# Kernel optimization log

Measured on AMD Instinct MI355X. Metric: run time of the kernel, lower is better.

Reference implementation:

```python
import jax, jax.numpy as jnp
import numpy as np
from jax import lax

B, T = 2, 2
BT = B * T
C = 256
NH, DH = 8, 32
NL, NP = 3, 4
NLAYERS = 6
DFF = 1024
SHAPES = [(16, 16), (32, 32), (64, 64)]  # coarse -> fine, last is finest
STARTS = [0, 256, 1280]
LQ = 5376
H4 = W4 = 128
EPS = 1e-5


def setup_inputs():
    key = jax.random.key(0)
    ks = iter(jax.random.split(key, 64))
    def nrm(shape, s=0.02):
        return jax.random.normal(next(ks), shape, jnp.float32) * s
    inp = {}
    for l, (H, W) in enumerate(SHAPES):
        inp[f"src{l}"] = jax.random.normal(next(ks), (BT, C, H, W), jnp.float32)
        inp[f"pos{l}"] = jax.random.normal(next(ks), (BT, C, H, W), jnp.float32)
    inp["mask_features"] = jax.random.normal(next(ks), (B, C, T, H4, W4), jnp.float32)
    inp["level_embed"] = nrm((NL, C), 1.0)
    inp["off_w"] = nrm((NLAYERS, C, NH * NL * NP * 2), 0.01)
    inp["off_b"] = nrm((NLAYERS, NH * NL * NP * 2), 0.1)
    inp["aw_w"] = nrm((NLAYERS, C, NH * NL * NP))
    inp["aw_b"] = jnp.zeros((NLAYERS, NH * NL * NP), jnp.float32)
    inp["val_w"] = nrm((NLAYERS, C, C), 0.05)
    inp["val_b"] = jnp.zeros((NLAYERS, C), jnp.float32)
    inp["out_w"] = nrm((NLAYERS, C, C), 0.05)
    inp["out_b"] = jnp.zeros((NLAYERS, C), jnp.float32)
    inp["ln1_g"] = jnp.ones((NLAYERS, C), jnp.float32)
    inp["ln1_b"] = jnp.zeros((NLAYERS, C), jnp.float32)
    inp["ff1_w"] = nrm((NLAYERS, C, DFF))
    inp["ff1_b"] = jnp.zeros((NLAYERS, DFF), jnp.float32)
    inp["ff2_w"] = nrm((NLAYERS, DFF, C))
    inp["ff2_b"] = jnp.zeros((NLAYERS, C), jnp.float32)
    inp["ln2_g"] = jnp.ones((NLAYERS, C), jnp.float32)
    inp["ln2_b"] = jnp.zeros((NLAYERS, C), jnp.float32)
    inp["lat_w"] = nrm((NLAYERS, C, C, 1, 1), 0.05)
    inp["lat_b"] = jnp.zeros((NLAYERS, C), jnp.float32)
    inp["outc_w"] = nrm((NLAYERS, C, C, 3, 3), 0.02)
    inp["outc_b"] = jnp.zeros((NLAYERS, C), jnp.float32)
    return inp


def _ln(x, g, b):
    m = x.mean(-1, keepdims=True)
    v = ((x - m) ** 2).mean(-1, keepdims=True)
    return (x - m) * lax.rsqrt(v + EPS) * g + b


def _conv(x, w, b, pad):
    y = lax.conv_general_dilated(x, w, (1, 1), [(pad, pad), (pad, pad)],
                                 dimension_numbers=("NCHW", "OIHW", "NCHW"))
    return y + b[None, :, None, None]


def _sample_level(v_l, loc, H, W):
    # v_l: (BT, NH, H*W, DH); loc: (BT, LQ, NH, NP, 2) normalized [0,1]
    # grid_sample bilinear, align_corners=False, zero padding:
    # pixel coord = loc * size - 0.5
    bt, nh, _, dh = v_l.shape
    x = loc[..., 0] * W - 0.5
    y = loc[..., 1] * H - 0.5
    x0 = jnp.floor(x)
    y0 = jnp.floor(y)
    x0i = x0.astype(jnp.int32)
    y0i = y0.astype(jnp.int32)
    fx = (x - x0).transpose(0, 2, 1, 3)[..., None]  # (BT,NH,LQ,NP,1)
    fy = (y - y0).transpose(0, 2, 1, 3)[..., None]
    def gather(ix, iy):
        valid = (ix >= 0) & (ix < W) & (iy >= 0) & (iy < H)
        idx = jnp.clip(iy, 0, H - 1) * W + jnp.clip(ix, 0, W - 1)
        idx = idx.transpose(0, 2, 1, 3)  # (BT,NH,LQ,NP)
        Lq, P = idx.shape[2], idx.shape[3]
        g = jnp.take_along_axis(v_l, idx.reshape(bt, nh, Lq * P)[..., None], axis=2)
        g = g.reshape(bt, nh, Lq, P, dh)
        return g * valid.transpose(0, 2, 1, 3)[..., None]
    v00 = gather(x0i, y0i)
    v01 = gather(x0i + 1, y0i)
    v10 = gather(x0i, y0i + 1)
    v11 = gather(x0i + 1, y0i + 1)
    return (v00 * (1 - fx) * (1 - fy) + v01 * fx * (1 - fy)
            + v10 * (1 - fx) * fy + v11 * fx * fy)


def _ref_points():
    pts = []
    for (H, W) in SHAPES:
        ys = (jnp.arange(H, dtype=jnp.float32) + 0.5) / H
        xs = (jnp.arange(W, dtype=jnp.float32) + 0.5) / W
        gy, gx = jnp.meshgrid(ys, xs, indexing="ij")
        pts.append(jnp.stack([gx.reshape(-1), gy.reshape(-1)], -1))
    return jnp.concatenate(pts, 0)  # (LQ, 2); valid_ratios are all ones


def reference(src0, src1, src2, pos0, pos1, pos2, mask_features, level_embed,
              off_w, off_b, aw_w, aw_b, val_w, val_b, out_w, out_b,
              ln1_g, ln1_b, ff1_w, ff1_b, ff2_w, ff2_b, ln2_g, ln2_b,
              lat_w, lat_b, outc_w, outc_b):
    srcs = [src0, src1, src2]
    poss = [pos0, pos1, pos2]
    output = jnp.concatenate([s.reshape(BT, C, -1).transpose(0, 2, 1) for s in srcs], 1)
    posf = jnp.concatenate(
        [p.reshape(BT, C, -1).transpose(0, 2, 1) + level_embed[l][None, None]
         for l, p in enumerate(poss)], 1)
    refp = _ref_points()
    norm = jnp.array([[W, H] for (H, W) in SHAPES], jnp.float32)  # (NL,2) as (W,H)
    lh, lw = SHAPES[-1]
    for i in range(NLAYERS):
        q = output + posf
        v = (output @ val_w[i] + val_b[i]).reshape(BT, LQ, NH, DH)
        off = (q @ off_w[i] + off_b[i]).reshape(BT, LQ, NH, NL, NP, 2)
        aw = jax.nn.softmax((q @ aw_w[i] + aw_b[i]).reshape(BT, LQ, NH, NL * NP), -1)
        aw = aw.reshape(BT, LQ, NH, NL, NP)
        loc = refp[None, :, None, None, None, :] + off / norm[None, None, None, :, None, :]
        acc = jnp.zeros((BT, NH, LQ, DH), output.dtype)
        for l, (H, W) in enumerate(SHAPES):
            v_l = v[:, STARTS[l]:STARTS[l] + H * W].transpose(0, 2, 1, 3)
            s = _sample_level(v_l, loc[:, :, :, l], H, W)
            acc = acc + (s * aw[:, :, :, l].transpose(0, 2, 1, 3)[..., None]).sum(3)
        attn = acc.transpose(0, 2, 1, 3).reshape(BT, LQ, C) @ out_w[i] + out_b[i]
        output = _ln(output + attn, ln1_g[i], ln1_b[i])
        ff = jax.nn.relu(output @ ff1_w[i] + ff1_b[i]) @ ff2_w[i] + ff2_b[i]
        output = _ln(output + ff, ln2_g[i], ln2_b[i])
        # FPN fusion with the finest transformer level
        lm = output[:, STARTS[-1]:].reshape(BT, lh, lw, C).transpose(0, 3, 1, 2)
        x = mask_features.transpose(0, 2, 1, 3, 4).reshape(B * T, C, H4, W4)
        x = _conv(x, lat_w[i], lat_b[i], 0)
        x = x + jax.image.resize(lm, (BT, C, H4, W4), method="bilinear")
        x = jax.nn.relu(_conv(x, outc_w[i], outc_b[i], 1))
        mask_features = mask_features + x.reshape(B, T, C, H4, W4).transpose(0, 2, 1, 3, 4)
    return output, mask_features
```

## Files before the change

kernel.cpp:

```cpp
#include <hip/hip_runtime.h>

#define DEV __device__ __forceinline__

using f32x4  = __attribute__((ext_vector_type(4))) float;
using bf16x8 = __attribute__((ext_vector_type(8))) short;

static constexpr int kLQ = 5376;

DEV unsigned short f2b(float f) {
  unsigned u = __builtin_bit_cast(unsigned, f);
  u = u + 0x7fffu + ((u >> 16) & 1u);
  return (unsigned short)(u >> 16);
}
DEV float b2f(unsigned short s) {
  unsigned u = ((unsigned)s) << 16;
  return __builtin_bit_cast(float, u);
}

DEV void glds16(const void* g, void* l) {
  __builtin_amdgcn_global_load_lds(
      (const __attribute__((address_space(1))) void*)g,
      (__attribute__((address_space(3))) void*)l, 16, 0, 0);
}

template<int EPI>
__global__ __launch_bounds__(256) void gemm128(
    const unsigned short* __restrict__ A, const unsigned short* __restrict__ Bt,
    const float* __restrict__ bias, void* __restrict__ Cp,
    int M, int N, int K, const float* __restrict__ rsrc)
{
  __shared__ unsigned short As[128 * 32];
  __shared__ unsigned short Bs[128 * 32];
  const int tid = threadIdx.x, lane = tid & 63, wid = tid >> 6;
  const int m0 = blockIdx.x * 128, n0 = blockIdx.y * 128;
  const int wr = wid >> 1, wc = wid & 1;
  const int l15 = lane & 15, lg = lane >> 4;

  const int s0 = wid * 64 + lane, s1 = 256 + s0;
  const int r0 = s0 >> 2, cs0 = (s0 & 3) ^ ((r0 >> 1) & 3);
  const int r1 = s1 >> 2, cs1 = (s1 & 3) ^ ((r1 >> 1) & 3);
  const unsigned short* Ag0 = A + (long)(m0 + r0) * K + cs0 * 8;
  const unsigned short* Ag1 = A + (long)(m0 + r1) * K + cs1 * 8;
  const unsigned short* Bg0 = Bt + (long)(n0 + r0) * K + cs0 * 8;
  const unsigned short* Bg1 = Bt + (long)(n0 + r1) * K + cs1 * 8;
  unsigned short* Al0 = As + (wid * 64) * 8;
  unsigned short* Al1 = As + (256 + wid * 64) * 8;
  unsigned short* Bl0 = Bs + (wid * 64) * 8;
  unsigned short* Bl1 = Bs + (256 + wid * 64) * 8;

  f32x4 acc[4][4];
#pragma unroll
  for (int i = 0; i < 4; i++)
#pragma unroll
    for (int j = 0; j < 4; j++) acc[i][j] = f32x4{0.f, 0.f, 0.f, 0.f};

  for (int k0 = 0; k0 < K; k0 += 32) {
    glds16(Ag0 + k0, Al0);
    glds16(Ag1 + k0, Al1);
    glds16(Bg0 + k0, Bl0);
    glds16(Bg1 + k0, Bl1);
    __syncthreads();
    bf16x8 a[4], b[4];
#pragma unroll
    for (int i = 0; i < 4; i++) {
      int ra = wr * 64 + i * 16 + l15;
      a[i] = *(const bf16x8*)(As + ra * 32 + (lg ^ ((ra >> 1) & 3)) * 8);
      int rb = wc * 64 + i * 16 + l15;
      b[i] = *(const bf16x8*)(Bs + rb * 32 + (lg ^ ((rb >> 1) & 3)) * 8);
    }
#pragma unroll
    for (int mi = 0; mi < 4; mi++)
#pragma unroll
      for (int nj = 0; nj < 4; nj++)
        acc[mi][nj] = __builtin_amdgcn_mfma_f32_16x16x32_bf16(
            a[mi], b[nj], acc[mi][nj], 0, 0, 0);
    __syncthreads();
  }

  int ry0 = 0, ry1 = 0;
  float rfy = 0.f;
  const float* rb0 = nullptr;
  if (EPI == 3) {
    const int bt = m0 >> 14, y = (m0 & 16383) >> 7;
    float sy = y * 0.5f - 0.25f;
    float y0f = floorf(sy);
    rfy = sy - y0f;
    ry0 = min(63, max(0, (int)y0f));
    ry1 = min(63, max(0, (int)y0f + 1));
    rb0 = rsrc + ((long)bt * kLQ + 1280) * 256;
  }

#pragma unroll
  for (int mi = 0; mi < 4; mi++)
#pragma unroll
    for (int nj = 0; nj < 4; nj++) {
      int col = n0 + wc * 64 + nj * 16 + l15;
      if (col >= N) continue;
      float bb = bias[col];
#pragma unroll
      for (int rr = 0; rr < 4; rr++) {
        long row = m0 + wr * 64 + mi * 16 + lg * 4 + rr;
        float v = acc[mi][nj][rr] + bb;
        if (EPI == 2) v = fmaxf(v, 0.f);
        if (EPI == 3) {
          int x = wr * 64 + mi * 16 + lg * 4 + rr;
          float sx = x * 0.5f - 0.25f;
          float x0f = floorf(sx);
          float fx = sx - x0f;
          int x0 = min(63, max(0, (int)x0f)), x1 = min(63, max(0, (int)x0f + 1));
          float v00 = rb0[(long)(ry0 * 64 + x0) * 256 + col];
          float v01 = rb0[(long)(ry0 * 64 + x1) * 256 + col];
          float v10 = rb0[(long)(ry1 * 64 + x0) * 256 + col];
          float v11 = rb0[(long)(ry1 * 64 + x1) * 256 + col];
          v += (1.f - rfy) * ((1.f - fx) * v00 + fx * v01)
             + rfy * ((1.f - fx) * v10 + fx * v11);
        }
        if (EPI == 0) ((float*)Cp)[row * N + col] = v;
        else ((unsigned short*)Cp)[row * N + col] = f2b(v);
      }
    }
}

__global__ __launch_bounds__(256) void conv3x3(
    const unsigned short* __restrict__ xb, const unsigned short* __restrict__ wT,
    const float* __restrict__ bias, float* __restrict__ mf,
    unsigned short* __restrict__ mc)
{
  __shared__ unsigned short As[128 * 32];
  __shared__ unsigned short Bs[128 * 32];
  const int tid = threadIdx.x, lane = tid & 63, wid = tid >> 6;
  const int y = blockIdx.x, c0 = blockIdx.y * 128, bt = blockIdx.z;
  const int wr = wid >> 1, wc = wid & 1;
  const int l15 = lane & 15, lg = lane >> 4;

  const int sA0 = tid, sA1 = 256 + tid;
  const int ax0 = sA0 >> 2, acl0 = (sA0 & 3) ^ ((ax0 >> 1) & 3);
  const int ax1 = sA1 >> 2, acl1 = (sA1 & 3) ^ ((ax1 >> 1) & 3);
  const int sB0 = wid * 64 + lane, sB1 = 256 + sB0;
  const int bc0 = sB0 >> 2, bcl0 = (sB0 & 3) ^ ((bc0 >> 1) & 3);
  const int bc1 = sB1 >> 2, bcl1 = (sB1 & 3) ^ ((bc1 >> 1) & 3);
  unsigned short* Bl0 = Bs + (wid * 64) * 8;
  unsigned short* Bl1 = Bs + (256 + wid * 64) * 8;
  const unsigned short* xbb = xb + (long)bt * (16384 * 256);

  f32x4 acc[4][4];
#pragma unroll
  for (int i = 0; i < 4; i++)
#pragma unroll
    for (int j = 0; j < 4; j++) acc[i][j] = f32x4{0.f, 0.f, 0.f, 0.f};

  for (int s = 0; s < 72; s++) {
    const int t = s >> 3, ci0 = (s & 7) * 32;
    const int dy = t / 3 - 1, dx = t % 3 - 1;
    const int yy = y + dy;
    uint4 av0 = {0u, 0u, 0u, 0u}, av1 = {0u, 0u, 0u, 0u};
    const int xx0 = ax0 + dx, xx1 = ax1 + dx;
    if ((unsigned)yy < 128u) {
      if ((unsigned)xx0 < 128u)
        av0 = *(const uint4*)(xbb + ((long)(yy * 128 + xx0)) * 256 + ci0 + acl0 * 8);
      if ((unsigned)xx1 < 128u)
        av1 = *(const uint4*)(xbb + ((long)(yy * 128 + xx1)) * 256 + ci0 + acl1 * 8);
    }
    *(uint4*)(As + sA0 * 8) = av0;
    *(uint4*)(As + sA1 * 8) = av1;
    glds16(wT + ((long)(c0 + bc0) * 9 + t) * 256 + ci0 + bcl0 * 8, Bl0);
    glds16(wT + ((long)(c0 + bc1) * 9 + t) * 256 + ci0 + bcl1 * 8, Bl1);
    __syncthreads();
    bf16x8 a[4], b[4];
#pragma unroll
    for (int i = 0; i < 4; i++) {
      int ra = wr * 64 + i * 16 + l15;
      a[i] = *(const bf16x8*)(As + ra * 32 + (lg ^ ((ra >> 1) & 3)) * 8);
      int rb = wc * 64 + i * 16 + l15;
      b[i] = *(const bf16x8*)(Bs + rb * 32 + (lg ^ ((rb >> 1) & 3)) * 8);
    }
#pragma unroll
    for (int mi = 0; mi < 4; mi++)
#pragma unroll
      for (int nj = 0; nj < 4; nj++)
        acc[mi][nj] = __builtin_amdgcn_mfma_f32_16x16x32_bf16(
            a[mi], b[nj], acc[mi][nj], 0, 0, 0);
    __syncthreads();
  }

#pragma unroll
  for (int mi = 0; mi < 4; mi++)
#pragma unroll
    for (int nj = 0; nj < 4; nj++) {
      int co = c0 + wc * 64 + nj * 16 + l15;
      float bb = bias[co];
#pragma unroll
      for (int rr = 0; rr < 4; rr++) {
        int x = wr * 64 + mi * 16 + lg * 4 + rr;
        long idx = ((long)bt * 16384 + y * 128 + x) * 256 + co;
        float v = mf[idx] + fmaxf(acc[mi][nj][rr] + bb, 0.f);
        mf[idx] = v;
        mc[idx] = f2b(v);
      }
    }
}

__global__ __launch_bounds__(256) void deform_sample(
    const float* __restrict__ offp, const float* __restrict__ awlog,
    const unsigned short* __restrict__ vp, unsigned short* __restrict__ attn)
{
  const int m = blockIdx.x * 4 + (threadIdx.x >> 6);
  const int t = threadIdx.x & 63;
  const int h = t >> 3, d4 = t & 7;
  const int bt = m / kLQ, q = m % kLQ;
  int pq, Wq;
  if (q < 256)       { pq = q;        Wq = 16; }
  else if (q < 1280) { pq = q - 256;  Wq = 32; }
  else               { pq = q - 1280; Wq = 64; }
  const float refx = ((pq % Wq) + 0.5f) / Wq;
  const float refy = ((pq / Wq) + 0.5f) / Wq;
  const int starts[3] = {0, 256, 1280};
  const int dims[3]   = {16, 32, 64};

  const float4* offr = (const float4*)(offp + (long)m * 192 + h * 24);
  const float4* awr  = (const float4*)(awlog + (long)m * 96 + h * 12);
  float off[24], aw[12];
#pragma unroll
  for (int j = 0; j < 6; j++) {
    float4 v = offr[j];
    off[j * 4] = v.x; off[j * 4 + 1] = v.y; off[j * 4 + 2] = v.z; off[j * 4 + 3] = v.w;
  }
#pragma unroll
  for (int j = 0; j < 3; j++) {
    float4 v = awr[j];
    aw[j * 4] = v.x; aw[j * 4 + 1] = v.y; aw[j * 4 + 2] = v.z; aw[j * 4 + 3] = v.w;
  }
  float mx = aw[0];
#pragma unroll
  for (int j = 1; j < 12; j++) mx = fmaxf(mx, aw[j]);
  float ssum = 0.f;
#pragma unroll
  for (int j = 0; j < 12; j++) { float e = __expf(aw[j] - mx); aw[j] = e; ssum += e; }
  float inv = 1.f / ssum;

  const unsigned short* vb = vp + ((long)bt * kLQ) * 256 + h * 32 + d4 * 4;
  float ax = 0.f, ay = 0.f, az = 0.f, aww = 0.f;
#pragma unroll
  for (int l = 0; l < 3; l++) {
    const int Wl = dims[l];
    const float winv = 1.f / (float)Wl;
    const int st = starts[l];
#pragma unroll
    for (int p = 0; p < 4; p++) {
      float ox = off[l * 8 + p * 2], oy = off[l * 8 + p * 2 + 1];
      float a  = aw[l * 4 + p] * inv;
      float fxp = (refx + ox * winv) * Wl - 0.5f;
      float fyp = (refy + oy * winv) * Wl - 0.5f;
      float x0f = floorf(fxp), y0f = floorf(fyp);
      int x0 = (int)x0f, y0 = (int)y0f;
      float fx = fxp - x0f, fy = fyp - y0f;
      float sx = 0.f, sy = 0.f, sz = 0.f, sw = 0.f;
#pragma unroll
      for (int cy = 0; cy < 2; cy++)
#pragma unroll
        for (int cx = 0; cx < 2; cx++) {
          int ix = x0 + cx, iy = y0 + cy;
          if ((unsigned)ix < (unsigned)Wl && (unsigned)iy < (unsigned)Wl) {
            float w = (cx ? fx : 1.f - fx) * (cy ? fy : 1.f - fy);
            ushort4 u = *(const ushort4*)(vb + (long)(st + iy * Wl + ix) * 256);
            sx += w * b2f(u.x); sy += w * b2f(u.y);
            sz += w * b2f(u.z); sw += w * b2f(u.w);
          }
        }
      ax += a * sx; ay += a * sy; az += a * sz; aww += a * sw;
    }
  }
  ushort4 r;
  r.x = f2b(ax); r.y = f2b(ay); r.z = f2b(az); r.w = f2b(aww);
  *(ushort4*)(attn + (long)m * 256 + h * 32 + d4 * 4) = r;
}

template<bool QB>
__global__ __launch_bounds__(256) void ln_row(
    float* __restrict__ out, const float* __restrict__ delta,
    const float* __restrict__ g, const float* __restrict__ b,
    unsigned short* __restrict__ ob, const float* __restrict__ posf,
    unsigned short* __restrict__ qb)
{
  const long m = blockIdx.x * 4 + (threadIdx.x >> 6);
  const int lane = threadIdx.x & 63;
  const long base = m * 256 + lane * 4;
  float4 a = *(const float4*)(out + base);
  float4 d = *(const float4*)(delta + base);
  float x0 = a.x + d.x, x1 = a.y + d.y, x2 = a.z + d.z, x3 = a.w + d.w;
  float s = x0 + x1 + x2 + x3;
#pragma unroll
  for (int o = 32; o > 0; o >>= 1) s += __shfl_xor(s, o);
  float mean = s * (1.f / 256.f);
  float d0 = x0 - mean, d1 = x1 - mean, d2 = x2 - mean, d3 = x3 - mean;
  float s2 = d0 * d0 + d1 * d1 + d2 * d2 + d3 * d3;
#pragma unroll
  for (int o = 32; o > 0; o >>= 1) s2 += __shfl_xor(s2, o);
  float rs = rsqrtf(s2 * (1.f / 256.f) + 1e-5f);
  float4 gv = *(const float4*)(g + lane * 4);
  float4 bv = *(const float4*)(b + lane * 4);
  float r0 = d0 * rs * gv.x + bv.x, r1 = d1 * rs * gv.y + bv.y;
  float r2 = d2 * rs * gv.z + bv.z, r3 = d3 * rs * gv.w + bv.w;
  *(float4*)(out + base) = float4{r0, r1, r2, r3};
  ushort4 o4; o4.x = f2b(r0); o4.y = f2b(r1); o4.z = f2b(r2); o4.w = f2b(r3);
  *(ushort4*)(ob + base) = o4;
  if (QB) {
    float4 pf = *(const float4*)(posf + base);
    ushort4 q4;
    q4.x = f2b(r0 + pf.x); q4.y = f2b(r1 + pf.y);
    q4.z = f2b(r2 + pf.z); q4.w = f2b(r3 + pf.w);
    *(ushort4*)(qb + base) = q4;
  }
}

__global__ __launch_bounds__(256) void wtrans_pad(
    const float* __restrict__ in, unsigned short* __restrict__ outT,
    int K, int N, int Npad)
{
  int idx = blockIdx.x * 256 + threadIdx.x;
  if (idx >= Npad * K) return;
  int n = idx / K, k = idx % K;
  unsigned short v = 0;
  if (n < N) v = f2b(in[(long)blockIdx.z * K * N + (long)k * N + n]);
  outT[(long)blockIdx.z * Npad * K + idx] = v;
}

__global__ __launch_bounds__(256) void wconvert(
    const float* __restrict__ in, unsigned short* __restrict__ out, int n)
{
  int idx = blockIdx.x * 256 + threadIdx.x;
  if (idx < n) out[idx] = f2b(in[idx]);
}

__global__ __launch_bounds__(256) void wpermconv(
    const float* __restrict__ in, unsigned short* __restrict__ out)
{
  int idx = blockIdx.x * 256 + threadIdx.x;
  const int ci = idx & 255;
  const int t  = (idx >> 8) % 9;
  const int co = ((idx >> 8) / 9) % 256;
  const int l  = idx / (256 * 9 * 256);
  out[idx] = f2b(in[(((long)l * 256 + co) * 256 + ci) * 9 + t]);
}

__global__ __launch_bounds__(256) void init_level(
    const float* __restrict__ src, const float* __restrict__ pos,
    const float* __restrict__ emb, float* __restrict__ outp,
    float* __restrict__ posf, unsigned short* __restrict__ ob,
    unsigned short* __restrict__ qb, int HW, int start)
{
  __shared__ float t1[32][33];
  __shared__ float t2[32][33];
  const int bt = blockIdx.z;
  const int p0 = blockIdx.x * 32, c0 = blockIdx.y * 32;
  const int tx = threadIdx.x, ty = threadIdx.y;
  const float* sb = src + ((long)bt * 256 + c0) * HW + p0;
  const float* pb = pos + ((long)bt * 256 + c0) * HW + p0;
#pragma unroll
  for (int j = 0; j < 4; j++) {
    int cc = ty + j * 8;
    t1[cc][tx] = sb[(long)cc * HW + tx];
    t2[cc][tx] = pb[(long)cc * HW + tx];
  }
  __syncthreads();
#pragma unroll
  for (int j = 0; j < 4; j++) {
    int pp = ty + j * 8;
    long row = (long)bt * kLQ + start + p0 + pp;
    float v = t1[tx][pp];
    float pv = t2[tx][pp] + emb[c0 + tx];
    outp[row * 256 + c0 + tx] = v;
    ob[row * 256 + c0 + tx] = f2b(v);
    qb[row * 256 + c0 + tx] = f2b(v + pv);
    posf[row * 256 + c0 + tx] = pv;
  }
}

__global__ __launch_bounds__(256) void init_mask(
    const float* __restrict__ in, float* __restrict__ mf,
    unsigned short* __restrict__ mc)
{
  __shared__ float t[32][33];
  const int bt = blockIdx.z, b = bt >> 1, tt = bt & 1;
  const int p0 = blockIdx.x * 32, c0 = blockIdx.y * 32;
  const int tx = threadIdx.x, ty = threadIdx.y;
  const float* base = in + (((long)b * 256 + c0) * 2 + tt) * 16384 + p0;
#pragma unroll
  for (int j = 0; j < 4; j++) {
    int cc = ty + j * 8;
    t[cc][tx] = base[(long)cc * 32768 + tx];
  }
  __syncthreads();
#pragma unroll
  for (int j = 0; j < 4; j++) {
    int pp = ty + j * 8;
    long idx = ((long)bt * 16384 + p0 + pp) * 256 + c0 + tx;
    float v = t[tx][pp];
    mf[idx] = v;
    mc[idx] = f2b(v);
  }
}

__global__ __launch_bounds__(256) void hwc_to_out(
    const float* __restrict__ mf, float* __restrict__ outm)
{
  __shared__ float t[32][33];
  const int bt = blockIdx.z, b = bt >> 1, tt = bt & 1;
  const int p0 = blockIdx.x * 32, c0 = blockIdx.y * 32;
  const int tx = threadIdx.x, ty = threadIdx.y;
#pragma unroll
  for (int j = 0; j < 4; j++) {
    int pp = ty + j * 8;
    t[pp][tx] = mf[((long)bt * 16384 + p0 + pp) * 256 + c0 + tx];
  }
  __syncthreads();
#pragma unroll
  for (int j = 0; j < 4; j++) {
    int cc = ty + j * 8;
    outm[(((long)b * 256 + c0 + cc) * 2 + tt) * 16384 + p0 + tx] = t[tx][cc];
  }
}

extern "C" void kernel_launch(void* const* d_in, const int* in_sizes, int n_in,
                              void* d_out, int out_size, void* d_ws, size_t ws_size,
                              hipStream_t stream)
{
  const float* src[3] = {(const float*)d_in[0], (const float*)d_in[2], (const float*)d_in[4]};
  const float* pos[3] = {(const float*)d_in[1], (const float*)d_in[3], (const float*)d_in[5]};
  const float* mask_in = (const float*)d_in[6];
  const float* lemb    = (const float*)d_in[7];
  const float* off_w   = (const float*)d_in[8];
  const float* off_b   = (const float*)d_in[9];
  const float* aw_w    = (const float*)d_in[10];
  const float* aw_b    = (const float*)d_in[11];
  const float* val_w   = (const float*)d_in[12];
  const float* val_b   = (const float*)d_in[13];
  const float* out_w   = (const float*)d_in[14];
  const float* out_b   = (const float*)d_in[15];
  const float* ln1_g   = (const float*)d_in[16];
  const float* ln1_b   = (const float*)d_in[17];
  const float* ff1_w   = (const float*)d_in[18];
  const float* ff1_b   = (const float*)d_in[19];
  const float* ff2_w   = (const float*)d_in[20];
  const float* ff2_b   = (const float*)d_in[21];
  const float* ln2_g   = (const float*)d_in[22];
  const float* ln2_b   = (const float*)d_in[23];
  const float* lat_w   = (const float*)d_in[24];
  const float* lat_b   = (const float*)d_in[25];
  const float* outc_w  = (const float*)d_in[26];
  const float* outc_b  = (const float*)d_in[27];

  float* outbuf = (float*)d_out;
  float* maskf  = (float*)d_out + 5505024;

  char* wp = (char*)d_ws;
  auto alloc = [&](size_t bytes) {
    char* p = wp;
    wp += (bytes + 255) & ~(size_t)255;
    return p;
  };
  float*          posf  = (float*)alloc(5505024ull * 4);
  unsigned short* qb    = (unsigned short*)alloc(5505024ull * 2);
  unsigned short* ob    = (unsigned short*)alloc(5505024ull * 2);
  unsigned short* vbuf  = (unsigned short*)alloc(5505024ull * 2);
  float*          offb  = (float*)alloc(4128768ull * 4);
  float*          awb   = (float*)alloc(2064384ull * 4);
  unsigned short* attnb = (unsigned short*)alloc(5505024ull * 2);
  float*          tmp1  = (float*)alloc(5505024ull * 4);
  unsigned short* ffh   = (unsigned short*)alloc(22020096ull * 2);
  unsigned short* mc    = (unsigned short*)alloc(16777216ull * 2);
  unsigned short* xb    = (unsigned short*)alloc(16777216ull * 2);
  float*          mfh   = (float*)alloc(16777216ull * 4);
  unsigned short* valT  = (unsigned short*)alloc(6ull * 65536 * 2);
  unsigned short* offT  = (unsigned short*)alloc(6ull * 65536 * 2);
  unsigned short* awT   = (unsigned short*)alloc(6ull * 32768 * 2);
  unsigned short* outT  = (unsigned short*)alloc(6ull * 65536 * 2);
  unsigned short* ff1T  = (unsigned short*)alloc(6ull * 262144 * 2);
  unsigned short* ff2T  = (unsigned short*)alloc(6ull * 262144 * 2);
  unsigned short* latT  = (unsigned short*)alloc(6ull * 65536 * 2);
  unsigned short* outcT = (unsigned short*)alloc(6ull * 589824 * 2);

  wtrans_pad<<<dim3(256, 1, 6), 256, 0, stream>>>(val_w, valT, 256, 256, 256);
  wtrans_pad<<<dim3(256, 1, 6), 256, 0, stream>>>(off_w, offT, 256, 192, 256);
  wtrans_pad<<<dim3(128, 1, 6), 256, 0, stream>>>(aw_w,  awT,  256, 96, 128);
  wtrans_pad<<<dim3(256, 1, 6), 256, 0, stream>>>(out_w, outT, 256, 256, 256);
  wtrans_pad<<<dim3(1024, 1, 6), 256, 0, stream>>>(ff1_w, ff1T, 256, 1024, 1024);
  wtrans_pad<<<dim3(1024, 1, 6), 256, 0, stream>>>(ff2_w, ff2T, 1024, 256, 256);
  wconvert<<<dim3(1536), 256, 0, stream>>>(lat_w, latT, 6 * 65536);
  wpermconv<<<dim3(13824), 256, 0, stream>>>(outc_w, outcT);

  const int hw[3] = {256, 1024, 4096};
  const int st[3] = {0, 256, 1280};
  for (int l = 0; l < 3; l++)
    init_level<<<dim3(hw[l] / 32, 8, 4), dim3(32, 8), 0, stream>>>(
        src[l], pos[l], lemb + l * 256, outbuf, posf, ob, qb, hw[l], st[l]);
  init_mask<<<dim3(512, 8, 4), dim3(32, 8), 0, stream>>>(mask_in, mfh, mc);

  for (int i = 0; i < 6; i++) {
    gemm128<1><<<dim3(168, 2), 256, 0, stream>>>(
        ob, valT + (long)i * 65536, val_b + i * 256, vbuf, 21504, 256, 256, nullptr);
    gemm128<0><<<dim3(168, 2), 256, 0, stream>>>(
        qb, offT + (long)i * 65536, off_b + i * 192, offb, 21504, 192, 256, nullptr);
    gemm128<0><<<dim3(168, 1), 256, 0, stream>>>(
        qb, awT + (long)i * 32768, aw_b + i * 96, awb, 21504, 96, 256, nullptr);
    deform_sample<<<dim3(5376), 256, 0, stream>>>(offb, awb, vbuf, attnb);
    gemm128<0><<<dim3(168, 2), 256, 0, stream>>>(
        attnb, outT + (long)i * 65536, out_b + i * 256, tmp1, 21504, 256, 256, nullptr);
    ln_row<false><<<dim3(5376), 256, 0, stream>>>(
        outbuf, tmp1, ln1_g + i * 256, ln1_b + i * 256, ob, nullptr, nullptr);
    gemm128<2><<<dim3(168, 8), 256, 0, stream>>>(
        ob, ff1T + (long)i * 262144, ff1_b + i * 1024, ffh, 21504, 1024, 256, nullptr);
    gemm128<0><<<dim3(168, 2), 256, 0, stream>>>(
        ffh, ff2T + (long)i * 262144, ff2_b + i * 256, tmp1, 21504, 256, 1024, nullptr);
    ln_row<true><<<dim3(5376), 256, 0, stream>>>(
        outbuf, tmp1, ln2_g + i * 256, ln2_b + i * 256, ob, posf, qb);
    gemm128<3><<<dim3(512, 2), 256, 0, stream>>>(
        mc, latT + (long)i * 65536, lat_b + i * 256, xb, 65536, 256, 256, outbuf);
    conv3x3<<<dim3(128, 2, 4), 256, 0, stream>>>(
        xb, outcT + (long)i * 589824, outc_b + i * 256, mfh, mc);
  }
  hwc_to_out<<<dim3(512, 8, 4), dim3(32, 8), 0, stream>>>(mfh, maskf);
}
```

Measured before the change: 3.069 ms.

## Stage three input rows once per channel slice and reuse across 3x3 taps

Result: faster. 2.828 ms (-7.8%).

```diff
diff --git a/kernel.cpp b/kernel.cpp
--- a/kernel.cpp
+++ b/kernel.cpp
@@ -126,22 +126,13 @@
     const float* __restrict__ bias, float* __restrict__ mf,
     unsigned short* __restrict__ mc)
 {
-  __shared__ unsigned short As[128 * 32];
-  __shared__ unsigned short Bs[128 * 32];
+  __shared__ unsigned short As[3 * 128 * 32];
   const int tid = threadIdx.x, lane = tid & 63, wid = tid >> 6;
   const int y = blockIdx.x, c0 = blockIdx.y * 128, bt = blockIdx.z;
   const int wr = wid >> 1, wc = wid & 1;
   const int l15 = lane & 15, lg = lane >> 4;
-
-  const int sA0 = tid, sA1 = 256 + tid;
-  const int ax0 = sA0 >> 2, acl0 = (sA0 & 3) ^ ((ax0 >> 1) & 3);
-  const int ax1 = sA1 >> 2, acl1 = (sA1 & 3) ^ ((ax1 >> 1) & 3);
-  const int sB0 = wid * 64 + lane, sB1 = 256 + sB0;
-  const int bc0 = sB0 >> 2, bcl0 = (sB0 & 3) ^ ((bc0 >> 1) & 3);
-  const int bc1 = sB1 >> 2, bcl1 = (sB1 & 3) ^ ((bc1 >> 1) & 3);
-  unsigned short* Bl0 = Bs + (wid * 64) * 8;
-  unsigned short* Bl1 = Bs + (256 + wid * 64) * 8;
   const unsigned short* xbb = xb + (long)bt * (16384 * 256);
+  const bool zr0 = (y == 0), zr2 = (y == 127);
 
   f32x4 acc[4][4];
 #pragma unroll
@@ -149,37 +140,48 @@
 #pragma unroll
     for (int j = 0; j < 4; j++) acc[i][j] = f32x4{0.f, 0.f, 0.f, 0.f};
 
-  for (int s = 0; s < 72; s++) {
-    const int t = s >> 3, ci0 = (s & 7) * 32;
-    const int dy = t / 3 - 1, dx = t % 3 - 1;
-    const int yy = y + dy;
-    uint4 av0 = {0u, 0u, 0u, 0u}, av1 = {0u, 0u, 0u, 0u};
-    const int xx0 = ax0 + dx, xx1 = ax1 + dx;
-    if ((unsigned)yy < 128u) {
-      if ((unsigned)xx0 < 128u)
-        av0 = *(const uint4*)(xbb + ((long)(yy * 128 + xx0)) * 256 + ci0 + acl0 * 8);
-      if ((unsigned)xx1 < 128u)
-        av1 = *(const uint4*)(xbb + ((long)(yy * 128 + xx1)) * 256 + ci0 + acl1 * 8);
+  for (int s = 0; s < 8; s++) {
+    const int ci0 = s * 32;
+#pragma unroll
+    for (int k = 0; k < 6; k++) {
+      const int S = k * 256 + tid;
+      const int r = S >> 9;
+      const int p = (S >> 2) & 127;
+      const int cs = (S & 3) ^ ((p >> 1) & 3);
+      if ((r == 0 && zr0) || (r == 2 && zr2)) {
+        *(uint4*)(As + S * 8) = uint4{0u, 0u, 0u, 0u};
+      } else {
+        glds16(xbb + ((long)((y + r - 1) * 128 + p) * 256 + ci0 + cs * 8),
+               As + (k * 256 + wid * 64) * 8);
+      }
     }
-    *(uint4*)(As + sA0 * 8) = av0;
-    *(uint4*)(As + sA1 * 8) = av1;
-    glds16(wT + ((long)(c0 + bc0) * 9 + t) * 256 + ci0 + bcl0 * 8, Bl0);
-    glds16(wT + ((long)(c0 + bc1) * 9 + t) * 256 + ci0 + bcl1 * 8, Bl1);
     __syncthreads();
-    bf16x8 a[4], b[4];
-#pragma unroll
-    for (int i = 0; i < 4; i++) {
-      int ra = wr * 64 + i * 16 + l15;
-      a[i] = *(const bf16x8*)(As + ra * 32 + (lg ^ ((ra >> 1) & 3)) * 8);
-      int rb = wc * 64 + i * 16 + l15;
-      b[i] = *(const bf16x8*)(Bs + rb * 32 + (lg ^ ((rb >> 1) & 3)) * 8);
+#pragma unroll
+    for (int r = 0; r < 3; r++) {
+#pragma unroll
+      for (int dxi = 0; dxi < 3; dxi++) {
+        const int t = r * 3 + dxi, dx = dxi - 1;
+        const unsigned short* wb = wT + (((long)t * 8 + s) * 256) * 32;
+        bf16x8 a[4], b[4];
+#pragma unroll
+        for (int i = 0; i < 4; i++) {
+          const int co_r = c0 + wc * 64 + i * 16 + l15;
+          b[i] = *(const bf16x8*)(wb + co_r * 32 + lg * 8);
+          const int px = wr * 64 + i * 16 + l15 + dx;
+          const int pxc = min(127, max(0, px));
+          bf16x8 v = *(const bf16x8*)(
+              As + ((r * 128 + pxc) * 4 + (lg ^ ((pxc >> 1) & 3))) * 8);
+          if ((unsigned)px >= 128u) v = bf16x8{0, 0, 0, 0, 0, 0, 0, 0};
+          a[i] = v;
+        }
+#pragma unroll
+        for (int mi = 0; mi < 4; mi++)
+#pragma unroll
+          for (int nj = 0; nj < 4; nj++)
+            acc[mi][nj] = __builtin_amdgcn_mfma_f32_16x16x32_bf16(
+                a[mi], b[nj], acc[mi][nj], 0, 0, 0);
+      }
     }
-#pragma unroll
-    for (int mi = 0; mi < 4; mi++)
-#pragma unroll
-      for (int nj = 0; nj < 4; nj++)
-        acc[mi][nj] = __builtin_amdgcn_mfma_f32_16x16x32_bf16(
-            a[mi], b[nj], acc[mi][nj], 0, 0, 0);
     __syncthreads();
   }
 
@@ -337,10 +339,12 @@
 {
   int idx = blockIdx.x * 256 + threadIdx.x;
   const int ci = idx & 255;
-  const int t  = (idx >> 8) % 9;
-  const int co = ((idx >> 8) / 9) % 256;
-  const int l  = idx / (256 * 9 * 256);
-  out[idx] = f2b(in[(((long)l * 256 + co) * 256 + ci) * 9 + t]);
+  const int co = (idx >> 8) & 255;
+  const int t  = (idx >> 16) % 9;
+  const int l  = idx / (9 << 16);
+  const int s = ci >> 5, cin = ci & 31;
+  out[((((long)l * 9 + t) * 8 + s) * 256 + co) * 32 + cin] =
+      f2b(in[(((long)l * 256 + co) * 256 + ci) * 9 + t]);
 }
 
 __global__ __launch_bounds__(256) void init_level(
```
